# Kernel tuning notes

Measured on AMD Instinct MI355X. Metric: run time of the kernel, lower is better.

## Reference

```python
import jax, jax.numpy as jnp
import numpy as np

HIDDEN = 128
POOL = 64
G = 4            # grid_size
NBHD = 2.0       # neighborhood_size (meters)
NUM_SCENES = 256
PEDS = 64        # pedestrians per scene (uniform seq_start_end)


def setup_inputs() -> dict:
    key = jax.random.key(0)
    k1, k2, k3 = jax.random.split(key, 3)
    hidden_states = jax.random.normal(k1, (NUM_SCENES * PEDS, HIDDEN), jnp.float32)
    positions = jax.random.uniform(k2, (NUM_SCENES * PEDS, 2), jnp.float32)
    fan_in = HIDDEN * G * G
    weight = jax.random.normal(k3, (fan_in, POOL), jnp.float32) / np.sqrt(fan_in)
    bias = jnp.zeros((POOL,), jnp.float32)
    return {
        "hidden_states": hidden_states,
        "positions": positions,
        "weight": weight,
        "bias": bias,
        "peds_per_scene": PEDS,
    }


def reference(hidden_states, positions, weight, bias, peds_per_scene):
    total, H = hidden_states.shape
    P = peds_per_scene
    B = total // P
    h = hidden_states.reshape(B, P, H)
    p = positions.reshape(B, P, 2)

    # rel[b, i, j] = pos[j] - pos[i]  (matches curr_pos - curr_pos[i:i+1])
    rel = p[:, None, :, :] - p[:, :, None, :]            # [B, P, P, 2]
    in_range = (jnp.abs(rel[..., 0]) <= NBHD) & (jnp.abs(rel[..., 1]) <= NBHD)
    not_self = ~jnp.eye(P, dtype=bool)[None]
    mask = in_range & not_self                            # [B, P, P]

    # int() truncation == floor here since (rel + NBHD) >= 0 inside the range check
    scale = G / (2.0 * NBHD)
    gx = jnp.clip(jnp.floor((rel[..., 0] + NBHD) * scale).astype(jnp.int32), 0, G - 1)
    gy = jnp.clip(jnp.floor((rel[..., 1] + NBHD) * scale).astype(jnp.int32), 0, G - 1)
    grid_idx = gy * G + gx                                # [B, P, P]

    # scatter-add of neighbor hidden states into G*G bins via masked one-hot
    onehot = jax.nn.one_hot(grid_idx, G * G, dtype=h.dtype) * mask[..., None].astype(h.dtype)
    grid = jnp.einsum('bijg,bjh->bigh', onehot, h)        # [B, P, G*G, H]

    flat = grid.reshape(B * P, G * G * H)                 # row-major: (grid_idx, hidden)
    return flat @ weight + bias                            # [total_peds, POOL]
```

## Files before the change

kernel.cpp:

```cpp
#include <hip/hip_runtime.h>
#include <cstdint>

#define HIDDEN 128
#define POOL   64
#define GRIDG  4
#define NBHD   2.0f
#define PEDS   64

typedef unsigned short u16;
typedef unsigned int   u32;
typedef __attribute__((ext_vector_type(8))) short bf16x8;
typedef __attribute__((ext_vector_type(4))) float f32x4;

__device__ __forceinline__ u16 f2bf(float f) {
    u32 u = __float_as_uint(f);
    u += 0x7fffu + ((u >> 16) & 1u);
    return (u16)(u >> 16);
}
__device__ __forceinline__ u32 pack2bf(float a, float b) {
    return (u32)f2bf(a) | ((u32)f2bf(b) << 16);
}
__device__ __forceinline__ float bflo(u32 u){ return __uint_as_float(u << 16); }
__device__ __forceinline__ float bfhi(u32 u){ return __uint_as_float(u & 0xffff0000u); }

__global__ __launch_bounds__(256) void social_pool_fused(
    const float* __restrict__ h, const float* __restrict__ pos,
    const float* __restrict__ w, const float* __restrict__ bias,
    float* __restrict__ out)
{
    __shared__ u16 LDS[32768];
    const int s    = blockIdx.x;
    const int tid  = threadIdx.x;
    const int lane = tid & 63;
    const int wv   = tid >> 6;
    const int l15  = lane & 15;
    const int q    = lane >> 4;

    float px = pos[((size_t)s * PEDS + lane) * 2 + 0];
    float py = pos[((size_t)s * PEDS + lane) * 2 + 1];

    const int hrow = tid >> 2;
    const int hq   = tid & 3;
    const float* hsrc = h + ((size_t)s * PEDS + hrow) * HIDDEN + hq * 32;
    float4 hv[8];
#pragma unroll
    for (int e = 0; e < 8; ++e) hv[e] = ((const float4*)hsrc)[e];

    const int i  = tid >> 2;
    const int jo = tid & 3;
    const float pxi = __shfl(px, i);
    const float pyi = __shfl(py, i);
    u32 gw[4] = {0u, 0u, 0u, 0u};
    unsigned um = 0u;
    const float scale = (float)GRIDG / (2.0f * NBHD);
#pragma unroll
    for (int u = 0; u < 16; ++u) {
        int j = jo * 16 + u;
        float rx = __shfl(px, j) - pxi;
        float ry = __shfl(py, j) - pyi;
        u32 gb = 0xffu;
        if ((i != j) && (fabsf(rx) <= NBHD) && (fabsf(ry) <= NBHD)) {
            int gx = (int)floorf((rx + NBHD) * scale); gx = min(max(gx, 0), GRIDG - 1);
            int gy = (int)floorf((ry + NBHD) * scale); gy = min(max(gy, 0), GRIDG - 1);
            int g = gy * GRIDG + gx;
            gb = (u32)g;
            um |= 1u << g;
        }
        gw[u >> 2] |= gb << ((u & 3) * 8);
    }

    unsigned* maskPtr = (unsigned*)&LDS[16384];
    if (tid == 0) *maskPtr = 0u;

#pragma unroll
    for (int cc = 0; cc < 4; ++cc) {
        float4 f0 = hv[cc * 2], f1 = hv[cc * 2 + 1];
        u32 p0 = pack2bf(f0.x, f0.y);
        u32 p1 = pack2bf(f0.z, f0.w);
        u32 p2 = pack2bf(f1.x, f1.y);
        u32 p3 = pack2bf(f1.z, f1.w);
        *(uint4*)&LDS[hrow * 128 + (((hq * 4 + cc) ^ (hrow & 15)) << 3)] =
            make_uint4(p0, p1, p2, p3);
    }
    __syncthreads();

    atomicOr(maskPtr, um);

    bf16x8 af[4];
    const int arow = wv * 16 + l15;
#pragma unroll
    for (int st4 = 0; st4 < 4; ++st4)
        af[st4] = *(const bf16x8*)&LDS[arow * 128 + (((st4 * 4 + q) ^ l15) << 3)];

    __syncthreads();
    const unsigned mask = *maskPtr;

    *(uint4*)&LDS[tid * 8] = make_uint4(gw[0], gw[1], gw[2], gw[3]);
    __syncthreads();

    u32 gr[16];
#pragma unroll
    for (int p = 0; p < 4; ++p) {
        uint4 qv = *(const uint4*)&LDS[i * 32 + p * 8];
        gr[p * 4 + 0] = qv.x; gr[p * 4 + 1] = qv.y;
        gr[p * 4 + 2] = qv.z; gr[p * 4 + 3] = qv.w;
    }

    float a0[8], a1[8];
#pragma unroll
    for (int e = 0; e < 8; ++e) { a0[e] = 0.f; a1[e] = 0.f; }

    unsigned rem = mask;
    int bi = 0;
    while (rem) {
        for (int t = 0; t < 4; ++t) {
            if (!rem) break;
            int g = __ffs(rem) - 1;
            rem &= rem - 1u;

            {
                const int r_ = lane;
                const int kq = wv;
                const float* src = w + ((size_t)g * 128 + kq * 32) * 64 + r_;
                float v[32];
#pragma unroll
                for (int e = 0; e < 32; ++e) v[e] = src[(size_t)e * 64];
#pragma unroll
                for (int cc = 0; cc < 4; ++cc) {
                    u32 p0 = pack2bf(v[cc * 8 + 0], v[cc * 8 + 1]);
                    u32 p1 = pack2bf(v[cc * 8 + 2], v[cc * 8 + 3]);
                    u32 p2 = pack2bf(v[cc * 8 + 4], v[cc * 8 + 5]);
                    u32 p3 = pack2bf(v[cc * 8 + 6], v[cc * 8 + 7]);
                    *(uint4*)&LDS[8192 + r_ * 128 + (((kq * 4 + cc) ^ (r_ & 15)) << 3)] =
                        make_uint4(p0, p1, p2, p3);
                }
            }
            __syncthreads();

            {
                f32x4 acc[4];
#pragma unroll
                for (int ni = 0; ni < 4; ++ni) acc[ni] = (f32x4){0.f, 0.f, 0.f, 0.f};
#pragma unroll
                for (int st4 = 0; st4 < 4; ++st4) {
                    bf16x8 bfrag[4];
#pragma unroll
                    for (int ni = 0; ni < 4; ++ni)
                        bfrag[ni] = *(const bf16x8*)&LDS[8192 + (ni * 16 + l15) * 128 +
                                                         (((st4 * 4 + q) ^ l15) << 3)];
#pragma unroll
                    for (int ni = 0; ni < 4; ++ni)
                        acc[ni] = __builtin_amdgcn_mfma_f32_16x16x32_bf16(
                            af[st4], bfrag[ni], acc[ni], 0, 0, 0);
                }
#pragma unroll
                for (int ni = 0; ni < 4; ++ni) {
                    int c = ni * 16 + l15;
                    int o = c >> 3;
                    int cpos = ((o ^ t) << 3) + (c & 7);
#pragma unroll
                    for (int r = 0; r < 4; ++r) {
                        int jrow = wv * 16 + q * 4 + r;
                        LDS[16384 + t * 4096 + jrow * 64 + cpos] = f2bf(acc[ni][r]);
                    }
                }
            }
            __syncthreads();
        }

#pragma unroll
        for (int p = 0; p < 16; ++p) {
            u32 gu = gr[p];
#pragma unroll
            for (int b = 0; b < 4; ++b) {
                int j = p * 4 + b;
                int g = (int)(signed char)(gu >> (b * 8));
                if (g >= 0) {
                    int slot = __popc(mask & ((1u << g) - 1u));
                    if ((slot >> 2) == bi) {
                        int st = slot & 3;
                        const u16* hb_ = &LDS[16384 + st * 4096 + j * 64];
                        uint4 r0 = *(const uint4*)(hb_ + ((jo ^ st) << 3));
                        uint4 r1 = *(const uint4*)(hb_ + (((jo + 4) ^ st) << 3));
                        a0[0] += bflo(r0.x); a0[1] += bfhi(r0.x);
                        a0[2] += bflo(r0.y); a0[3] += bfhi(r0.y);
                        a0[4] += bflo(r0.z); a0[5] += bfhi(r0.z);
                        a0[6] += bflo(r0.w); a0[7] += bfhi(r0.w);
                        a1[0] += bflo(r1.x); a1[1] += bfhi(r1.x);
                        a1[2] += bflo(r1.y); a1[3] += bfhi(r1.y);
                        a1[4] += bflo(r1.z); a1[5] += bfhi(r1.z);
                        a1[6] += bflo(r1.w); a1[7] += bfhi(r1.w);
                    }
                }
            }
        }
        __syncthreads();
        ++bi;
    }

    const size_t orow = ((size_t)s * PEDS + i) * POOL;
    {
        int oc = jo * 8;
        float4 bb0 = *(const float4*)&bias[oc];
        float4 bb1 = *(const float4*)&bias[oc + 4];
        *(float4*)&out[orow + oc] =
            make_float4(a0[0] + bb0.x, a0[1] + bb0.y, a0[2] + bb0.z, a0[3] + bb0.w);
        *(float4*)&out[orow + oc + 4] =
            make_float4(a0[4] + bb1.x, a0[5] + bb1.y, a0[6] + bb1.z, a0[7] + bb1.w);
    }
    {
        int oc = (jo + 4) * 8;
        float4 bb0 = *(const float4*)&bias[oc];
        float4 bb1 = *(const float4*)&bias[oc + 4];
        *(float4*)&out[orow + oc] =
            make_float4(a1[0] + bb0.x, a1[1] + bb0.y, a1[2] + bb0.z, a1[3] + bb0.w);
        *(float4*)&out[orow + oc + 4] =
            make_float4(a1[4] + bb1.x, a1[5] + bb1.y, a1[6] + bb1.z, a1[7] + bb1.w);
    }
}

extern "C" void kernel_launch(void* const* d_in, const int* in_sizes, int n_in,
                              void* d_out, int out_size, void* d_ws, size_t ws_size,
                              hipStream_t stream) {
    const float* h    = (const float*)d_in[0];
    const float* pos  = (const float*)d_in[1];
    const float* w    = (const float*)d_in[2];
    const float* bias = (const float*)d_in[3];
    float* out = (float*)d_out;

    const int total = in_sizes[0] / HIDDEN;
    const int B     = total / PEDS;

    hipLaunchKernelGGL(social_pool_fused, dim3(B), dim3(256), 0, stream,
                       h, pos, w, bias, out);
}
```

Measured before the change: 81.93 us.

## Replace scalar bin scatter with one-hot MFMA and double-buffer weight slices

Recasts the per-bin neighbor accumulation as a second MFMA, using a bf16 one-hot mask matrix built from the grid indices times the transposed H·W_g tile. This replaces the scalar loop that walked 64 neighbors with bf16 unpacking. The block grows to 512 threads split across M-tiles and N-halves. Weight slices for the next occupied bin are prefetched into registers while the current bin runs, using double-buffered LDS. The occupancy mask is reduced with wave shuffles instead of an LDS atomic. The larger 64KB LDS footprint and 512-thread blocks may cut the number of resident blocks per CU.

```diff
diff --git a/kernel.cpp b/kernel.cpp
--- a/kernel.cpp
+++ b/kernel.cpp
@@ -1,11 +1,11 @@
 #include <hip/hip_runtime.h>
 #include <cstdint>
 
+#define PEDS   64
 #define HIDDEN 128
 #define POOL   64
 #define GRIDG  4
 #define NBHD   2.0f
-#define PEDS   64
 
 typedef unsigned short u16;
 typedef unsigned int   u32;
@@ -20,202 +20,169 @@
 __device__ __forceinline__ u32 pack2bf(float a, float b) {
     return (u32)f2bf(a) | ((u32)f2bf(b) << 16);
 }
-__device__ __forceinline__ float bflo(u32 u){ return __uint_as_float(u << 16); }
-__device__ __forceinline__ float bfhi(u32 u){ return __uint_as_float(u & 0xffff0000u); }
-
-__global__ __launch_bounds__(256) void social_pool_fused(
+
+__global__ __launch_bounds__(512) void social_fused(
     const float* __restrict__ h, const float* __restrict__ pos,
     const float* __restrict__ w, const float* __restrict__ bias,
     float* __restrict__ out)
 {
-    __shared__ u16 LDS[32768];
+    __shared__ unsigned char LB[65536];
+    unsigned char* gidx  = LB;
+    u32*           wmask = (u32*)(LB + 4096);
+    u16*           hA    = (u16*)(LB + 8192);
+    u16*           hwT   = (u16*)(LB + 57344);
+
     const int s    = blockIdx.x;
     const int tid  = threadIdx.x;
+    const int wv   = tid >> 6;
     const int lane = tid & 63;
-    const int wv   = tid >> 6;
     const int l15  = lane & 15;
     const int q    = lane >> 4;
-
-    float px = pos[((size_t)s * PEDS + lane) * 2 + 0];
-    float py = pos[((size_t)s * PEDS + lane) * 2 + 1];
-
-    const int hrow = tid >> 2;
-    const int hq   = tid & 3;
-    const float* hsrc = h + ((size_t)s * PEDS + hrow) * HIDDEN + hq * 32;
-    float4 hv[8];
-#pragma unroll
-    for (int e = 0; e < 8; ++e) hv[e] = ((const float4*)hsrc)[e];
-
-    const int i  = tid >> 2;
-    const int jo = tid & 3;
-    const float pxi = __shfl(px, i);
-    const float pyi = __shfl(py, i);
-    u32 gw[4] = {0u, 0u, 0u, 0u};
-    unsigned um = 0u;
+    const int mt   = wv & 3;
+    const int nh   = wv >> 2;
+
+    float2 pp = ((const float2*)pos)[(size_t)s * PEDS + lane];
+    float px = pp.x, py = pp.y;
+
+    const int hrow = tid >> 3, hc = tid & 7;
+    const float4* hsrc = (const float4*)(h + ((size_t)s * PEDS + hrow) * HIDDEN + hc * 16);
+    float4 hv0 = hsrc[0], hv1 = hsrc[1], hv2 = hsrc[2], hv3 = hsrc[3];
+
+    const int gi  = wv * 8 + (lane >> 3);
+    const int gj0 = (lane & 7) * 8;
+    const float pxi = __shfl(px, gi), pyi = __shfl(py, gi);
+    u32 gpk0 = 0, gpk1 = 0, um = 0;
     const float scale = (float)GRIDG / (2.0f * NBHD);
 #pragma unroll
-    for (int u = 0; u < 16; ++u) {
-        int j = jo * 16 + u;
+    for (int u8 = 0; u8 < 8; ++u8) {
+        int j = gj0 + u8;
         float rx = __shfl(px, j) - pxi;
         float ry = __shfl(py, j) - pyi;
         u32 gb = 0xffu;
-        if ((i != j) && (fabsf(rx) <= NBHD) && (fabsf(ry) <= NBHD)) {
+        if ((gi != j) && (fabsf(rx) <= NBHD) && (fabsf(ry) <= NBHD)) {
             int gx = (int)floorf((rx + NBHD) * scale); gx = min(max(gx, 0), GRIDG - 1);
             int gy = (int)floorf((ry + NBHD) * scale); gy = min(max(gy, 0), GRIDG - 1);
             int g = gy * GRIDG + gx;
-            gb = (u32)g;
-            um |= 1u << g;
-        }
-        gw[u >> 2] |= gb << ((u & 3) * 8);
-    }
-
-    unsigned* maskPtr = (unsigned*)&LDS[16384];
-    if (tid == 0) *maskPtr = 0u;
-
-#pragma unroll
-    for (int cc = 0; cc < 4; ++cc) {
-        float4 f0 = hv[cc * 2], f1 = hv[cc * 2 + 1];
-        u32 p0 = pack2bf(f0.x, f0.y);
-        u32 p1 = pack2bf(f0.z, f0.w);
-        u32 p2 = pack2bf(f1.x, f1.y);
-        u32 p3 = pack2bf(f1.z, f1.w);
-        *(uint4*)&LDS[hrow * 128 + (((hq * 4 + cc) ^ (hrow & 15)) << 3)] =
-            make_uint4(p0, p1, p2, p3);
+            gb = (u32)g; um |= 1u << g;
+        }
+        if (u8 < 4) gpk0 |= gb << (u8 * 8); else gpk1 |= gb << ((u8 - 4) * 8);
+    }
+    *(uint2*)&gidx[gi * 64 + gj0] = make_uint2(gpk0, gpk1);
+
+#pragma unroll
+    for (int off = 32; off; off >>= 1) um |= __shfl_xor(um, off);
+    if (lane == 0) wmask[wv] = um;
+
+    {
+        u32 p0 = pack2bf(hv0.x, hv0.y), p1 = pack2bf(hv0.z, hv0.w);
+        u32 p2 = pack2bf(hv1.x, hv1.y), p3 = pack2bf(hv1.z, hv1.w);
+        int ch = hc * 2;
+        *(uint4*)&hA[hrow * 128 + ((ch ^ (hrow & 15)) << 3)] = make_uint4(p0, p1, p2, p3);
+        p0 = pack2bf(hv2.x, hv2.y); p1 = pack2bf(hv2.z, hv2.w);
+        p2 = pack2bf(hv3.x, hv3.y); p3 = pack2bf(hv3.z, hv3.w);
+        ch = hc * 2 + 1;
+        *(uint4*)&hA[hrow * 128 + ((ch ^ (hrow & 15)) << 3)] = make_uint4(p0, p1, p2, p3);
     }
     __syncthreads();
 
-    atomicOr(maskPtr, um);
+    u32 mask = wmask[0] | wmask[1] | wmask[2] | wmask[3]
+             | wmask[4] | wmask[5] | wmask[6] | wmask[7];
+    mask = __builtin_amdgcn_readfirstlane(mask);
 
     bf16x8 af[4];
-    const int arow = wv * 16 + l15;
 #pragma unroll
     for (int st4 = 0; st4 < 4; ++st4)
-        af[st4] = *(const bf16x8*)&LDS[arow * 128 + (((st4 * 4 + q) ^ l15) << 3)];
-
-    __syncthreads();
-    const unsigned mask = *maskPtr;
-
-    *(uint4*)&LDS[tid * 8] = make_uint4(gw[0], gw[1], gw[2], gw[3]);
-    __syncthreads();
-
-    u32 gr[16];
-#pragma unroll
-    for (int p = 0; p < 4; ++p) {
-        uint4 qv = *(const uint4*)&LDS[i * 32 + p * 8];
-        gr[p * 4 + 0] = qv.x; gr[p * 4 + 1] = qv.y;
-        gr[p * 4 + 2] = qv.z; gr[p * 4 + 3] = qv.w;
-    }
-
-    float a0[8], a1[8];
-#pragma unroll
-    for (int e = 0; e < 8; ++e) { a0[e] = 0.f; a1[e] = 0.f; }
-
-    unsigned rem = mask;
-    int bi = 0;
-    while (rem) {
-        for (int t = 0; t < 4; ++t) {
-            if (!rem) break;
-            int g = __ffs(rem) - 1;
-            rem &= rem - 1u;
-
-            {
-                const int r_ = lane;
-                const int kq = wv;
-                const float* src = w + ((size_t)g * 128 + kq * 32) * 64 + r_;
-                float v[32];
-#pragma unroll
-                for (int e = 0; e < 32; ++e) v[e] = src[(size_t)e * 64];
-#pragma unroll
-                for (int cc = 0; cc < 4; ++cc) {
-                    u32 p0 = pack2bf(v[cc * 8 + 0], v[cc * 8 + 1]);
-                    u32 p1 = pack2bf(v[cc * 8 + 2], v[cc * 8 + 3]);
-                    u32 p2 = pack2bf(v[cc * 8 + 4], v[cc * 8 + 5]);
-                    u32 p3 = pack2bf(v[cc * 8 + 6], v[cc * 8 + 7]);
-                    *(uint4*)&LDS[8192 + r_ * 128 + (((kq * 4 + cc) ^ (r_ & 15)) << 3)] =
-                        make_uint4(p0, p1, p2, p3);
-                }
+        af[st4] = *(const bf16x8*)&hA[(mt * 16 + l15) * 128 + (((st4 * 4 + q) ^ l15) << 3)];
+
+    const int ng = __popc(mask);
+    u32 rem = mask;
+    int g = 0;
+    if (rem) { g = __ffs(rem) - 1; rem &= rem - 1u; }
+
+    float wr[16];
+    const int wc = lane, wk = wv * 16;
+    if (ng) {
+        const float* wsrc = w + ((size_t)g * HIDDEN + wk) * POOL + wc;
+#pragma unroll
+        for (int e = 0; e < 16; ++e) wr[e] = wsrc[(size_t)e * POOL];
+    }
+
+    f32x4 oacc[2];
+    oacc[0] = (f32x4){0.f, 0.f, 0.f, 0.f};
+    oacc[1] = (f32x4){0.f, 0.f, 0.f, 0.f};
+
+    for (int t = 0; t < ng; ++t) {
+        u16* wSb = (u16*)(LB + 24576 + ((t & 1) << 14));
+#pragma unroll
+        for (int cc = 0; cc < 2; ++cc) {
+            u32 p0 = pack2bf(wr[cc * 8 + 0], wr[cc * 8 + 1]);
+            u32 p1 = pack2bf(wr[cc * 8 + 2], wr[cc * 8 + 3]);
+            u32 p2 = pack2bf(wr[cc * 8 + 4], wr[cc * 8 + 5]);
+            u32 p3 = pack2bf(wr[cc * 8 + 6], wr[cc * 8 + 7]);
+            int ch = wv * 2 + cc;
+            *(uint4*)&wSb[wc * 128 + ((ch ^ (wc & 15)) << 3)] = make_uint4(p0, p1, p2, p3);
+        }
+        int gn = -1;
+        if (rem) { gn = __ffs(rem) - 1; rem &= rem - 1u; }
+        if (gn >= 0) {
+            const float* wsrc = w + ((size_t)gn * HIDDEN + wk) * POOL + wc;
+#pragma unroll
+            for (int e = 0; e < 16; ++e) wr[e] = wsrc[(size_t)e * POOL];
+        }
+        __syncthreads();
+
+        f32x4 a1[2];
+        a1[0] = (f32x4){0.f, 0.f, 0.f, 0.f};
+        a1[1] = (f32x4){0.f, 0.f, 0.f, 0.f};
+#pragma unroll
+        for (int st4 = 0; st4 < 4; ++st4) {
+            int chs = ((st4 * 4 + q) ^ l15) << 3;
+            bf16x8 b0 = *(const bf16x8*)&wSb[(nh * 32 + l15) * 128 + chs];
+            bf16x8 b1 = *(const bf16x8*)&wSb[(nh * 32 + 16 + l15) * 128 + chs];
+            a1[0] = __builtin_amdgcn_mfma_f32_16x16x32_bf16(af[st4], b0, a1[0], 0, 0, 0);
+            a1[1] = __builtin_amdgcn_mfma_f32_16x16x32_bf16(af[st4], b1, a1[1], 0, 0, 0);
+        }
+#pragma unroll
+        for (int ni = 0; ni < 2; ++ni) {
+            int c = nh * 32 + ni * 16 + l15;
+            u32 lo = pack2bf(a1[ni][0], a1[ni][1]);
+            u32 hi = pack2bf(a1[ni][2], a1[ni][3]);
+            *(uint2*)&hwT[c * 64 + (((mt * 4 + q) ^ (c & 15)) << 2)] = make_uint2(lo, hi);
+        }
+        __syncthreads();
+
+#pragma unroll
+        for (int kk = 0; kk < 2; ++kk) {
+            uint2 gg = *(const uint2*)&gidx[(mt * 16 + l15) * 64 + kk * 32 + q * 8];
+            union { u16 hx[8]; bf16x8 v; } mu;
+#pragma unroll
+            for (int b = 0; b < 4; ++b)
+                mu.hx[b]     = (((gg.x >> (b * 8)) & 0xffu) == (u32)g) ? (u16)0x3F80 : (u16)0;
+#pragma unroll
+            for (int b = 0; b < 4; ++b)
+                mu.hx[4 + b] = (((gg.y >> (b * 8)) & 0xffu) == (u32)g) ? (u16)0x3F80 : (u16)0;
+#pragma unroll
+            for (int ni = 0; ni < 2; ++ni) {
+                int c = nh * 32 + ni * 16 + l15;
+                int cs = c & 15;
+                uint2 b0 = *(const uint2*)&hwT[c * 64 + (((kk * 8 + q * 2 + 0) ^ cs) << 2)];
+                uint2 b1 = *(const uint2*)&hwT[c * 64 + (((kk * 8 + q * 2 + 1) ^ cs) << 2)];
+                union { u32 u[4]; bf16x8 v; } bu;
+                bu.u[0] = b0.x; bu.u[1] = b0.y; bu.u[2] = b1.x; bu.u[3] = b1.y;
+                oacc[ni] = __builtin_amdgcn_mfma_f32_16x16x32_bf16(mu.v, bu.v, oacc[ni], 0, 0, 0);
             }
-            __syncthreads();
-
-            {
-                f32x4 acc[4];
-#pragma unroll
-                for (int ni = 0; ni < 4; ++ni) acc[ni] = (f32x4){0.f, 0.f, 0.f, 0.f};
-#pragma unroll
-                for (int st4 = 0; st4 < 4; ++st4) {
-                    bf16x8 bfrag[4];
-#pragma unroll
-                    for (int ni = 0; ni < 4; ++ni)
-                        bfrag[ni] = *(const bf16x8*)&LDS[8192 + (ni * 16 + l15) * 128 +
-                                                         (((st4 * 4 + q) ^ l15) << 3)];
-#pragma unroll
-                    for (int ni = 0; ni < 4; ++ni)
-                        acc[ni] = __builtin_amdgcn_mfma_f32_16x16x32_bf16(
-                            af[st4], bfrag[ni], acc[ni], 0, 0, 0);
-                }
-#pragma unroll
-                for (int ni = 0; ni < 4; ++ni) {
-                    int c = ni * 16 + l15;
-                    int o = c >> 3;
-                    int cpos = ((o ^ t) << 3) + (c & 7);
-#pragma unroll
-                    for (int r = 0; r < 4; ++r) {
-                        int jrow = wv * 16 + q * 4 + r;
-                        LDS[16384 + t * 4096 + jrow * 64 + cpos] = f2bf(acc[ni][r]);
-                    }
-                }
-            }
-            __syncthreads();
-        }
-
-#pragma unroll
-        for (int p = 0; p < 16; ++p) {
-            u32 gu = gr[p];
-#pragma unroll
-            for (int b = 0; b < 4; ++b) {
-                int j = p * 4 + b;
-                int g = (int)(signed char)(gu >> (b * 8));
-                if (g >= 0) {
-                    int slot = __popc(mask & ((1u << g) - 1u));
-                    if ((slot >> 2) == bi) {
-                        int st = slot & 3;
-                        const u16* hb_ = &LDS[16384 + st * 4096 + j * 64];
-                        uint4 r0 = *(const uint4*)(hb_ + ((jo ^ st) << 3));
-                        uint4 r1 = *(const uint4*)(hb_ + (((jo + 4) ^ st) << 3));
-                        a0[0] += bflo(r0.x); a0[1] += bfhi(r0.x);
-                        a0[2] += bflo(r0.y); a0[3] += bfhi(r0.y);
-                        a0[4] += bflo(r0.z); a0[5] += bfhi(r0.z);
-                        a0[6] += bflo(r0.w); a0[7] += bfhi(r0.w);
-                        a1[0] += bflo(r1.x); a1[1] += bfhi(r1.x);
-                        a1[2] += bflo(r1.y); a1[3] += bfhi(r1.y);
-                        a1[4] += bflo(r1.z); a1[5] += bfhi(r1.z);
-                        a1[6] += bflo(r1.w); a1[7] += bfhi(r1.w);
-                    }
-                }
-            }
-        }
-        __syncthreads();
-        ++bi;
-    }
-
-    const size_t orow = ((size_t)s * PEDS + i) * POOL;
-    {
-        int oc = jo * 8;
-        float4 bb0 = *(const float4*)&bias[oc];
-        float4 bb1 = *(const float4*)&bias[oc + 4];
-        *(float4*)&out[orow + oc] =
-            make_float4(a0[0] + bb0.x, a0[1] + bb0.y, a0[2] + bb0.z, a0[3] + bb0.w);
-        *(float4*)&out[orow + oc + 4] =
-            make_float4(a0[4] + bb1.x, a0[5] + bb1.y, a0[6] + bb1.z, a0[7] + bb1.w);
-    }
-    {
-        int oc = (jo + 4) * 8;
-        float4 bb0 = *(const float4*)&bias[oc];
-        float4 bb1 = *(const float4*)&bias[oc + 4];
-        *(float4*)&out[orow + oc] =
-            make_float4(a1[0] + bb0.x, a1[1] + bb0.y, a1[2] + bb0.z, a1[3] + bb0.w);
-        *(float4*)&out[orow + oc + 4] =
-            make_float4(a1[4] + bb1.x, a1[5] + bb1.y, a1[6] + bb1.z, a1[7] + bb1.w);
+        }
+        g = gn;
+    }
+
+#pragma unroll
+    for (int ni = 0; ni < 2; ++ni) {
+        int c = nh * 32 + ni * 16 + l15;
+        float bv = bias[c];
+        size_t ob = ((size_t)s * PEDS + mt * 16 + q * 4) * POOL + c;
+#pragma unroll
+        for (int r = 0; r < 4; ++r)
+            out[ob + (size_t)r * POOL] = oacc[ni][r] + bv;
     }
 }
 
@@ -231,6 +198,6 @@
     const int total = in_sizes[0] / HIDDEN;
     const int B     = total / PEDS;
 
-    hipLaunchKernelGGL(social_pool_fused, dim3(B), dim3(256), 0, stream,
+    hipLaunchKernelGGL(social_fused, dim3(B), dim3(512), 0, stream,
                        h, pos, w, bias, out);
 }
```

New measurement: 70.43 us. 1.16x faster.
